# Performance work log

Measured on AMD Instinct MI355X. Metric: run time of the kernel, lower is better.

## Reference

```python
import jax, jax.numpy as jnp
import numpy as np

N_NODES = 50000
N_EDGES = 800000
IN_DIM = 128
HID_DIM = 256
N_CLASS = 40
PROP_STEP = 3
DROPOUT = 0.0  # eval-mode drop_node scale = (1 - DROPOUT)


def setup_inputs() -> dict:
    key = jax.random.key(0)
    k = jax.random.split(key, 6)
    features = jax.random.normal(k[0], (N_NODES, IN_DIM), dtype=jnp.float32)
    src = jax.random.randint(k[1], (N_EDGES,), 0, N_NODES)
    dst = jax.random.randint(k[2], (N_EDGES,), 0, N_NODES)
    W1 = jax.random.normal(k[3], (IN_DIM, HID_DIM), dtype=jnp.float32) / np.sqrt(IN_DIM)
    b1 = jnp.zeros((HID_DIM,), dtype=jnp.float32)
    W2 = jax.random.normal(k[4], (HID_DIM, N_CLASS), dtype=jnp.float32) / np.sqrt(HID_DIM)
    b2 = jnp.zeros((N_CLASS,), dtype=jnp.float32)
    return {"features": features, "src": src, "dst": dst,
            "W1": W1, "b1": b1, "W2": W2, "b2": b2}


def reference(features, src, dst, W1, b1, W2, b2):
    N = features.shape[0]
    # in-degree-based symmetric normalization: norm = deg^{-1/2}, deg clamped to >= 1
    degs = jax.ops.segment_sum(jnp.ones_like(dst, dtype=jnp.float32), dst,
                               num_segments=N)
    norm = jnp.clip(degs, 1.0, None) ** -0.5              # [N]
    w = norm[src] * norm[dst]                             # [E] edge weights (u_mul_v)

    # eval-mode drop_node: scale features by (1 - drop_rate)
    x = features * (1.0 - DROPOUT)
    y = x
    for _ in range(PROP_STEP):
        # u_mul_e: gather source features, scale by edge weight, scatter-sum to dst
        m = x[src] * w[:, None]                           # [E, F]
        x = jax.ops.segment_sum(m, dst, num_segments=N)   # [N, F]
        y = y + x
    feat = y / (PROP_STEP + 1)

    # MLP (use_bn=False, dropouts are 0 / eval): relu(linear) -> linear
    h = jax.nn.relu(feat @ W1 + b1)
    logits = h @ W2 + b2
    return jax.nn.log_softmax(logits, axis=-1)
```

## Files before the change

kernel.cpp:

```cpp
#include <hip/hip_runtime.h>

#define IN_DIM 128
#define HID    256
#define NCLS   40
#define BSHIFT 8
#define BSZ    256
#define MAXNB  256
#define CHUNK  4096
#define CAP    5120

static inline size_t align256(size_t x) { return (x + 255) & ~(size_t)255; }

typedef __attribute__((ext_vector_type(2))) float f32x2;

__device__ inline unsigned pack_bf16x2(float x, float y) {
    unsigned xb = __float_as_uint(x), yb = __float_as_uint(y);
    unsigned lo = (xb + 0x7fffu + ((xb >> 16) & 1u)) >> 16;
    unsigned hi = (yb + 0x7fffu + ((yb >> 16) & 1u)) >> 16;
    return lo | (hi << 16);
}
__device__ inline unsigned short f2bf(float x) {
    unsigned b = __float_as_uint(x);
    return (unsigned short)((b + 0x7fffu + ((b >> 16) & 1u)) >> 16);
}

__device__ inline unsigned pack_fp8x4(float a, float b, float c, float d) {
    int v = __builtin_amdgcn_cvt_pk_fp8_f32(a, b, 0, false);
    v = __builtin_amdgcn_cvt_pk_fp8_f32(c, d, v, true);
    return (unsigned)v;
}

__global__ __launch_bounds__(256) void init_kernel(
        int* __restrict__ cursor,
        const float* __restrict__ W1, const float* __restrict__ W2,
        unsigned short* __restrict__ W1T, unsigned short* __restrict__ W2T) {
    int i = blockIdx.x * 256 + threadIdx.x;
    if (i < MAXNB) cursor[i] = i * CAP;
    if (i < 256 * 128) {
        int n = i >> 7, k = i & 127;
        W1T[i] = f2bf(W1[k * 256 + n]);
    }
    if (i < 48 * 256) {
        int c = i >> 8, kk = i & 255;
        W2T[i] = (c < 40) ? f2bf(W2[kk * 40 + c]) : (unsigned short)0;
    }
}

__global__ __launch_bounds__(256) void bucket_scatter_kernel(
        const int* __restrict__ src, const int* __restrict__ dst,
        int* __restrict__ bucketCursor, unsigned* __restrict__ ebuf, int E) {
    __shared__ int hist[MAXNB], lofs[MAXNB], lcur[MAXNB], gbase[MAXNB];
    __shared__ unsigned bin[CHUNK];
    int t = threadIdx.x, lane = t & 63, wave = t >> 6;
    int start = blockIdx.x * CHUNK;
    int cnt = min(CHUNK, E - start);
    hist[t] = 0;
    __syncthreads();
    for (int i = t; i < cnt; i += 256) atomicAdd(&hist[dst[start + i] >> BSHIFT], 1);
    __syncthreads();
    int v = hist[t];
    int s = v;
    for (int off = 1; off < 64; off <<= 1) {
        int u = __shfl_up(s, off, 64);
        if (lane >= off) s += u;
    }
    __shared__ int wsum[4];
    if (lane == 63) wsum[wave] = s;
    __syncthreads();
    if (t == 0) {
        int c = 0;
        for (int i = 0; i < 4; ++i) { int x = wsum[i]; wsum[i] = c; c += x; }
    }
    __syncthreads();
    int excl = wsum[wave] + s - v;
    lofs[t] = excl; lcur[t] = excl;
    if (v) gbase[t] = atomicAdd(&bucketCursor[t], v);
    __syncthreads();
    for (int i = t; i < cnt; i += 256) {
        unsigned s0 = (unsigned)src[start + i], d0 = (unsigned)dst[start + i];
        int b = d0 >> BSHIFT;
        int r = atomicAdd(&lcur[b], 1);
        bin[r] = ((unsigned)b << 24) | ((d0 & (BSZ - 1)) << 16) | s0;
    }
    __syncthreads();
    for (int i = t; i < cnt; i += 256) {
        unsigned e = bin[i];
        int b = e >> 24;
        ebuf[gbase[b] + i - lofs[b]] = e;
    }
}

__global__ __launch_bounds__(256) void bucketize_kernel(
        const unsigned* __restrict__ ebuf, const int* __restrict__ bucketCursor,
        int* __restrict__ offs, int* __restrict__ degs,
        float* __restrict__ norm, float* __restrict__ sqn,
        unsigned short* __restrict__ csrS, int N) {
    __shared__ unsigned sedge[CAP];
    __shared__ unsigned short sout[CAP];
    __shared__ int hist[BSZ], lcur[BSZ];
    __shared__ int wsum[4];
    int b = blockIdx.x, t = threadIdx.x, lane = t & 63, wave = t >> 6;
    int base = b * CAP;
    int cnt = bucketCursor[b] - base;
    hist[t] = 0;
    __syncthreads();
    for (int i = t; i < cnt; i += 256) {
        unsigned e = ebuf[base + i];
        sedge[i] = e;
        atomicAdd(&hist[(e >> 16) & (BSZ - 1)], 1);
    }
    __syncthreads();
    int v = hist[t];
    int s = v;
    for (int off = 1; off < 64; off <<= 1) {
        int u = __shfl_up(s, off, 64);
        if (lane >= off) s += u;
    }
    if (lane == 63) wsum[wave] = s;
    __syncthreads();
    if (t == 0) {
        int c = 0;
        for (int i = 0; i < 4; ++i) { int x = wsum[i]; wsum[i] = c; c += x; }
    }
    __syncthreads();
    int excl = wsum[wave] + s - v;
    lcur[t] = excl;
    int node = b * BSZ + t;
    if (node < N) {
        offs[node] = base + excl;
        degs[node] = v;
        float dc = (float)(v > 0 ? v : 1);
        norm[node] = rsqrtf(dc);
        sqn[node] = sqrtf(dc);
    }
    __syncthreads();
    for (int i = t; i < cnt; i += 256) {
        unsigned e = sedge[i];
        int ld = (e >> 16) & (BSZ - 1);
        int p = atomicAdd(&lcur[ld], 1);
        sout[p] = (unsigned short)(e & 0xffffu);
    }
    __syncthreads();
    for (int i = t; i < cnt; i += 256) csrS[base + i] = sout[i];
}

__global__ __launch_bounds__(256) void prep_kernel(
        const float* __restrict__ feat, const float* __restrict__ norm,
        unsigned* __restrict__ x0, int nfeat_dw) {
    int i = blockIdx.x * 256 + threadIdx.x;
    if (i >= nfeat_dw) return;
    float s = norm[i >> 5];
    float4 f = *(const float4*)(feat + (size_t)i * 4);
    x0[i] = pack_fp8x4(f.x * s, f.y * s, f.z * s, f.w * s);
}

#define ACCP16(dd, ww)                                                        \
    {                                                                         \
        f32x2 wv2 = {(ww), (ww)};                                             \
        c0 += __builtin_amdgcn_cvt_pk_f32_fp8((int)(dd).x, false) * wv2;      \
        c1 += __builtin_amdgcn_cvt_pk_f32_fp8((int)(dd).x, true ) * wv2;      \
        c2 += __builtin_amdgcn_cvt_pk_f32_fp8((int)(dd).y, false) * wv2;      \
        c3 += __builtin_amdgcn_cvt_pk_f32_fp8((int)(dd).y, true ) * wv2;      \
        c4 += __builtin_amdgcn_cvt_pk_f32_fp8((int)(dd).z, false) * wv2;      \
        c5 += __builtin_amdgcn_cvt_pk_f32_fp8((int)(dd).z, true ) * wv2;      \
        c6 += __builtin_amdgcn_cvt_pk_f32_fp8((int)(dd).w, false) * wv2;      \
        c7 += __builtin_amdgcn_cvt_pk_f32_fp8((int)(dd).w, true ) * wv2;      \
    }

#define RED2(a) { a += __shfl_xor(a, 8, 64); a += __shfl_xor(a, 16, 64); }

__global__ __launch_bounds__(256) void prop_kernel(
        const unsigned* __restrict__ xin, unsigned* __restrict__ xout,
        const int* __restrict__ offs, const int* __restrict__ degs,
        const float* __restrict__ norm, const unsigned short* __restrict__ csrS, int N) {
    int t = threadIdx.x;
    int wv = t >> 6, lane = t & 63;
    int h = lane >> 5, hl = lane & 31;
    int g = hl >> 3, gl = hl & 7;
    int v = blockIdx.x * 8 + wv * 2 + h;
    if (v >= N) return;
    int start = offs[v], end = start + degs[v];
    f32x2 c0 = {0.f,0.f}, c1 = {0.f,0.f}, c2 = {0.f,0.f}, c3 = {0.f,0.f};
    f32x2 c4 = {0.f,0.f}, c5 = {0.f,0.f}, c6 = {0.f,0.f}, c7 = {0.f,0.f};
    for (int k = start; k < end; k += 16) {
        int cnt = min(16, end - k);
        if (cnt == 16) {
            uint4 d[4];
#pragma unroll
            for (int u = 0; u < 4; ++u) {
                int sx = (int)csrS[k + 4 * u + g];
                d[u] = *(const uint4*)(xin + (size_t)sx * 32 + gl * 4);
            }
#pragma unroll
            for (int u = 0; u < 4; ++u) ACCP16(d[u], 1.0f);
        } else if (cnt > 8) {
            uint4 d[4]; float w[4];
#pragma unroll
            for (int u = 0; u < 4; ++u) {
                int il = 4 * u + g;
                int sx = (int)csrS[k + min(il, cnt - 1)];
                w[u] = (il < cnt) ? 1.f : 0.f;
                d[u] = *(const uint4*)(xin + (size_t)sx * 32 + gl * 4);
            }
#pragma unroll
            for (int u = 0; u < 4; ++u) ACCP16(d[u], w[u]);
        } else {
            uint4 d[2]; float w[2];
#pragma unroll
            for (int u = 0; u < 2; ++u) {
                int il = 4 * u + g;
                int sx = (int)csrS[k + min(il, cnt - 1)];
                w[u] = (il < cnt) ? 1.f : 0.f;
                d[u] = *(const uint4*)(xin + (size_t)sx * 32 + gl * 4);
            }
#pragma unroll
            for (int u = 0; u < 2; ++u) ACCP16(d[u], w[u]);
        }
    }
    float a0 = c0.x, a1 = c0.y, a2 = c1.x, a3 = c1.y;
    float a4 = c2.x, a5 = c2.y, a6 = c3.x, a7 = c3.y;
    float a8 = c4.x, a9 = c4.y, a10 = c5.x, a11 = c5.y;
    float a12 = c6.x, a13 = c6.y, a14 = c7.x, a15 = c7.y;
    RED2(a0); RED2(a1); RED2(a2); RED2(a3); RED2(a4); RED2(a5); RED2(a6); RED2(a7);
    RED2(a8); RED2(a9); RED2(a10); RED2(a11); RED2(a12); RED2(a13); RED2(a14); RED2(a15);
    if (g == 0) {
        float nv = norm[v];
        float s2 = nv * nv;
        uint4 o;
        o.x = pack_fp8x4(a0 * s2, a1 * s2, a2 * s2, a3 * s2);
        o.y = pack_fp8x4(a4 * s2, a5 * s2, a6 * s2, a7 * s2);
        o.z = pack_fp8x4(a8 * s2, a9 * s2, a10 * s2, a11 * s2);
        o.w = pack_fp8x4(a12 * s2, a13 * s2, a14 * s2, a15 * s2);
        *(uint4*)(xout + (size_t)v * 32 + gl * 4) = o;
    }
}

typedef __attribute__((ext_vector_type(8))) short bf16x8;
typedef __attribute__((ext_vector_type(4))) float f32x4;

#define SA_STRIDE 136
#define SH_STRIDE 264

__device__ inline void unpack8(uint2 u, float* q) {
    f32x2 p;
    p = __builtin_amdgcn_cvt_pk_f32_fp8((int)u.x, false); q[0] = p.x; q[1] = p.y;
    p = __builtin_amdgcn_cvt_pk_f32_fp8((int)u.x, true ); q[2] = p.x; q[3] = p.y;
    p = __builtin_amdgcn_cvt_pk_f32_fp8((int)u.y, false); q[4] = p.x; q[5] = p.y;
    p = __builtin_amdgcn_cvt_pk_f32_fp8((int)u.y, true ); q[6] = p.x; q[7] = p.y;
}

__global__ __launch_bounds__(256) void mlp16_kernel(
        const unsigned* __restrict__ x0, const unsigned* __restrict__ x1,
        const unsigned* __restrict__ x2, const unsigned* __restrict__ x3,
        const float* __restrict__ sqn,
        const unsigned short* __restrict__ W1T, const float* __restrict__ b1,
        const unsigned short* __restrict__ W2T, const float* __restrict__ b2,
        float* __restrict__ out, int N) {
    __shared__ unsigned short sA[16 * SA_STRIDE];
    __shared__ unsigned short sH[16 * SH_STRIDE];
    __shared__ float sLog[16][49];
    int t = threadIdx.x, wv = t >> 6, lane = t & 63;
    int l15 = lane & 15, lq = lane >> 4;
    int base = blockIdx.x * 16;

    {
        int n = t >> 4, sg = t & 15;
        int gv = base + n;
        uint4 o = make_uint4(0u, 0u, 0u, 0u);
        if (gv < N) {
            size_t xo = (size_t)gv * 32 + sg * 2;
            uint2 u0 = *(const uint2*)(x0 + xo);
            uint2 u1 = *(const uint2*)(x1 + xo);
            uint2 u2 = *(const uint2*)(x2 + xo);
            uint2 u3 = *(const uint2*)(x3 + xo);
            float q0[8], q1[8], q2[8], q3[8];
            unpack8(u0, q0); unpack8(u1, q1); unpack8(u2, q2); unpack8(u3, q3);
            float fac = 0.25f * sqn[gv];
            float s[8];
#pragma unroll
            for (int i = 0; i < 8; ++i) s[i] = (q0[i] + q1[i] + q2[i] + q3[i]) * fac;
            o.x = pack_bf16x2(s[0], s[1]); o.y = pack_bf16x2(s[2], s[3]);
            o.z = pack_bf16x2(s[4], s[5]); o.w = pack_bf16x2(s[6], s[7]);
        }
        *(uint4*)&sA[n * SA_STRIDE + sg * 8] = o;
    }
    __syncthreads();

    f32x4 acc[4];
#pragma unroll
    for (int ht = 0; ht < 4; ++ht) acc[ht] = (f32x4){0.f, 0.f, 0.f, 0.f};
#pragma unroll
    for (int s = 0; s < 4; ++s) {
        bf16x8 afr = *(const bf16x8*)&sA[l15 * SA_STRIDE + s * 32 + lq * 8];
#pragma unroll
        for (int ht = 0; ht < 4; ++ht) {
            bf16x8 bfr = *(const bf16x8*)(W1T + ((wv * 64 + ht * 16 + l15) * 128 + s * 32 + lq * 8));
            acc[ht] = __builtin_amdgcn_mfma_f32_16x16x32_bf16(afr, bfr, acc[ht], 0, 0, 0);
        }
    }
#pragma unroll
    for (int ht = 0; ht < 4; ++ht) {
        int hid = wv * 64 + ht * 16 + l15;
        float bb = b1[hid];
#pragma unroll
        for (int r = 0; r < 4; ++r) {
            int node = lq * 4 + r;
            sH[node * SH_STRIDE + hid] = f2bf(fmaxf(acc[ht][r] + bb, 0.f));
        }
    }
    __syncthreads();

    if (wv < 3) {
        int ct = wv;
        f32x4 acc2 = (f32x4){0.f, 0.f, 0.f, 0.f};
#pragma unroll
        for (int s = 0; s < 8; ++s) {
            bf16x8 afr = *(const bf16x8*)&sH[l15 * SH_STRIDE + s * 32 + lq * 8];
            bf16x8 bfr = *(const bf16x8*)(W2T + ((ct * 16 + l15) * 256 + s * 32 + lq * 8));
            acc2 = __builtin_amdgcn_mfma_f32_16x16x32_bf16(afr, bfr, acc2, 0, 0, 0);
        }
        int c = ct * 16 + l15;
        float bb = (c < NCLS) ? b2[c] : 0.f;
#pragma unroll
        for (int r = 0; r < 4; ++r) sLog[lq * 4 + r][c] = acc2[r] + bb;
    }
    __syncthreads();
    if (wv != 0) return;

    float lg[3][4];
#pragma unroll
    for (int ct = 0; ct < 3; ++ct)
#pragma unroll
        for (int r = 0; r < 4; ++r) lg[ct][r] = sLog[lq * 4 + r][ct * 16 + l15];
#pragma unroll
    for (int r = 0; r < 4; ++r) {
        float m = fmaxf(lg[0][r], lg[1][r]);
        if (l15 < 8) m = fmaxf(m, lg[2][r]);
        for (int off = 1; off < 16; off <<= 1) m = fmaxf(m, __shfl_xor(m, off, 64));
        float ssum = __expf(lg[0][r] - m) + __expf(lg[1][r] - m) +
                     ((l15 < 8) ? __expf(lg[2][r] - m) : 0.f);
        for (int off = 1; off < 16; off <<= 1) ssum += __shfl_xor(ssum, off, 64);
        float ls = m + __logf(ssum);
        int node = base + lq * 4 + r;
        if (node < N) {
#pragma unroll
            for (int ct = 0; ct < 3; ++ct) {
                int c = ct * 16 + l15;
                if (c < NCLS) out[(size_t)node * NCLS + c] = lg[ct][r] - ls;
            }
        }
    }
}

extern "C" void kernel_launch(void* const* d_in, const int* in_sizes, int n_in,
                              void* d_out, int out_size, void* d_ws, size_t ws_size,
                              hipStream_t stream) {
    const float* feat = (const float*)d_in[0];
    const int*   src  = (const int*)d_in[1];
    const int*   dst  = (const int*)d_in[2];
    const float* W1   = (const float*)d_in[3];
    const float* b1   = (const float*)d_in[4];
    const float* W2   = (const float*)d_in[5];
    const float* b2   = (const float*)d_in[6];
    float* out = (float*)d_out;

    int N = in_sizes[0] / IN_DIM;
    int E = in_sizes[1];
    int NB = (N + BSZ - 1) / BSZ;

    char* ws = (char*)d_ws;
    size_t off = 0;
    float* norm   = (float*)(ws + off); off += align256((size_t)N * 4);
    float* sqn    = (float*)(ws + off); off += align256((size_t)N * 4);
    int*   offs   = (int*)(ws + off);   off += align256((size_t)N * 4);
    int*   degs   = (int*)(ws + off);   off += align256((size_t)N * 4);
    int*   bCur   = (int*)(ws + off);   off += align256((size_t)MAXNB * 4);
    unsigned* ebuf = (unsigned*)(ws + off); off += align256((size_t)MAXNB * CAP * 4);
    unsigned short* csrS = (unsigned short*)(ws + off); off += align256((size_t)MAXNB * CAP * 2);
    unsigned* x0  = (unsigned*)(ws + off); off += align256((size_t)N * 32 * 4);
    unsigned* x1  = (unsigned*)(ws + off); off += align256((size_t)N * 32 * 4);
    unsigned* x2  = (unsigned*)(ws + off); off += align256((size_t)N * 32 * 4);
    unsigned* x3  = (unsigned*)(ws + off); off += align256((size_t)N * 32 * 4);
    unsigned short* W1T = (unsigned short*)(ws + off); off += align256((size_t)256 * 128 * 2);
    unsigned short* W2T = (unsigned short*)(ws + off); off += align256((size_t)48 * 256 * 2);
    (void)ws_size;

    init_kernel<<<128, 256, 0, stream>>>(bCur, W1, W2, W1T, W2T);

    int echunks = (E + CHUNK - 1) / CHUNK;
    bucket_scatter_kernel<<<echunks, 256, 0, stream>>>(src, dst, bCur, ebuf, E);
    bucketize_kernel<<<NB, 256, 0, stream>>>(ebuf, bCur, offs, degs, norm, sqn, csrS, N);

    prep_kernel<<<(N * 32 + 255) / 256, 256, 0, stream>>>(feat, norm, x0, N * 32);

    int pb = (N + 7) / 8;
    prop_kernel<<<pb, 256, 0, stream>>>(x0, x1, offs, degs, norm, csrS, N);
    prop_kernel<<<pb, 256, 0, stream>>>(x1, x2, offs, degs, norm, csrS, N);
    prop_kernel<<<pb, 256, 0, stream>>>(x2, x3, offs, degs, norm, csrS, N);

    mlp16_kernel<<<(N + 15) / 16, 256, 0, stream>>>(x0, x1, x2, x3, sqn,
                                                    W1T, b1, W2T, b2, out, N);
}
```

Measured before the change: 221.7 us.

## Fuse three propagation steps into a persistent kernel with grid barriers

Replaces the three separate prop_kernel launches with one persistent kernel of 1024 blocks that loops over node groups and uses an atomic-counter grid barrier between steps. It also folds the feature prep (norm scaling and fp8 packing) into the tail of the bucketize kernel. The aim is to remove launch overhead and inter-kernel gaps. In exchange, a spin-wait barrier is added that relies on all 1024 blocks being co-resident, which is a deadlock risk if occupancy is lower. The persistent grid-stride loop may also balance work less well than the full launch did.

```diff
diff --git a/kernel.cpp b/kernel.cpp
--- a/kernel.cpp
+++ b/kernel.cpp
@@ -8,10 +8,13 @@
 #define MAXNB  256
 #define CHUNK  4096
 #define CAP    5120
+#define P3GRID 1024
 
 static inline size_t align256(size_t x) { return (x + 255) & ~(size_t)255; }
 
 typedef __attribute__((ext_vector_type(2))) float f32x2;
+typedef __attribute__((ext_vector_type(8))) short bf16x8;
+typedef __attribute__((ext_vector_type(4))) float f32x4;
 
 __device__ inline unsigned pack_bf16x2(float x, float y) {
     unsigned xb = __float_as_uint(x), yb = __float_as_uint(y);
@@ -31,11 +34,12 @@
 }
 
 __global__ __launch_bounds__(256) void init_kernel(
-        int* __restrict__ cursor,
+        int* __restrict__ cursor, int* __restrict__ bar,
         const float* __restrict__ W1, const float* __restrict__ W2,
         unsigned short* __restrict__ W1T, unsigned short* __restrict__ W2T) {
     int i = blockIdx.x * 256 + threadIdx.x;
     if (i < MAXNB) cursor[i] = i * CAP;
+    if (i < 4) bar[i] = 0;
     if (i < 256 * 128) {
         int n = i >> 7, k = i & 127;
         W1T[i] = f2bf(W1[k * 256 + n]);
@@ -94,10 +98,12 @@
         const unsigned* __restrict__ ebuf, const int* __restrict__ bucketCursor,
         int* __restrict__ offs, int* __restrict__ degs,
         float* __restrict__ norm, float* __restrict__ sqn,
-        unsigned short* __restrict__ csrS, int N) {
+        unsigned short* __restrict__ csrS,
+        const float* __restrict__ feat, unsigned* __restrict__ x0, int N) {
     __shared__ unsigned sedge[CAP];
     __shared__ unsigned short sout[CAP];
     __shared__ int hist[BSZ], lcur[BSZ];
+    __shared__ float snorm[BSZ];
     __shared__ int wsum[4];
     int b = blockIdx.x, t = threadIdx.x, lane = t & 63, wave = t >> 6;
     int base = b * CAP;
@@ -126,13 +132,16 @@
     int excl = wsum[wave] + s - v;
     lcur[t] = excl;
     int node = b * BSZ + t;
+    float nv = 0.f;
     if (node < N) {
         offs[node] = base + excl;
         degs[node] = v;
         float dc = (float)(v > 0 ? v : 1);
-        norm[node] = rsqrtf(dc);
+        nv = rsqrtf(dc);
+        norm[node] = nv;
         sqn[node] = sqrtf(dc);
     }
+    snorm[t] = nv;
     __syncthreads();
     for (int i = t; i < cnt; i += 256) {
         unsigned e = sedge[i];
@@ -142,16 +151,18 @@
     }
     __syncthreads();
     for (int i = t; i < cnt; i += 256) csrS[base + i] = sout[i];
-}
-
-__global__ __launch_bounds__(256) void prep_kernel(
-        const float* __restrict__ feat, const float* __restrict__ norm,
-        unsigned* __restrict__ x0, int nfeat_dw) {
-    int i = blockIdx.x * 256 + threadIdx.x;
-    if (i >= nfeat_dw) return;
-    float s = norm[i >> 5];
-    float4 f = *(const float4*)(feat + (size_t)i * 4);
-    x0[i] = pack_fp8x4(f.x * s, f.y * s, f.z * s, f.w * s);
+
+    int nbase = b * BSZ;
+    int nvalid = min(BSZ, N - nbase);
+    if (nvalid <= 0) return;
+    int total = nvalid * 32;
+    const float4* f4 = (const float4*)(feat + (size_t)nbase * IN_DIM);
+    unsigned* xo = x0 + (size_t)nbase * 32;
+    for (int i = t; i < total; i += 256) {
+        float sc = snorm[i >> 5];
+        float4 f = f4[i];
+        xo[i] = pack_fp8x4(f.x * sc, f.y * sc, f.z * sc, f.w * sc);
+    }
 }
 
 #define ACCP16(dd, ww)                                                        \
@@ -169,74 +180,102 @@
 
 #define RED2(a) { a += __shfl_xor(a, 8, 64); a += __shfl_xor(a, 16, 64); }
 
-__global__ __launch_bounds__(256) void prop_kernel(
-        const unsigned* __restrict__ xin, unsigned* __restrict__ xout,
+__device__ inline void grid_barrier(int* bar, int slot, int nblk) {
+    __syncthreads();
+    if (threadIdx.x == 0) {
+        __threadfence();
+        atomicAdd(&bar[slot], 1);
+        while (__hip_atomic_load(&bar[slot], __ATOMIC_ACQUIRE,
+                                 __HIP_MEMORY_SCOPE_AGENT) < nblk) {
+            __builtin_amdgcn_s_sleep(1);
+        }
+        __threadfence();
+    }
+    __syncthreads();
+}
+
+__global__ __launch_bounds__(256, 4) void prop3_kernel(
+        const unsigned* __restrict__ x0, unsigned* __restrict__ x1,
+        unsigned* __restrict__ x2, unsigned* __restrict__ x3,
         const int* __restrict__ offs, const int* __restrict__ degs,
-        const float* __restrict__ norm, const unsigned short* __restrict__ csrS, int N) {
+        const float* __restrict__ norm, const unsigned short* __restrict__ csrS,
+        int* __restrict__ bar, int N) {
     int t = threadIdx.x;
     int wv = t >> 6, lane = t & 63;
     int h = lane >> 5, hl = lane & 31;
     int g = hl >> 3, gl = hl & 7;
-    int v = blockIdx.x * 8 + wv * 2 + h;
-    if (v >= N) return;
-    int start = offs[v], end = start + degs[v];
-    f32x2 c0 = {0.f,0.f}, c1 = {0.f,0.f}, c2 = {0.f,0.f}, c3 = {0.f,0.f};
-    f32x2 c4 = {0.f,0.f}, c5 = {0.f,0.f}, c6 = {0.f,0.f}, c7 = {0.f,0.f};
-    for (int k = start; k < end; k += 16) {
-        int cnt = min(16, end - k);
-        if (cnt == 16) {
-            uint4 d[4];
-#pragma unroll
-            for (int u = 0; u < 4; ++u) {
-                int sx = (int)csrS[k + 4 * u + g];
-                d[u] = *(const uint4*)(xin + (size_t)sx * 32 + gl * 4);
+    (void)hl;
+    int ngrp = (N + 7) >> 3;
+
+    const unsigned* xin = x0;
+    unsigned* xout = x1;
+    for (int step = 0; step < 3; ++step) {
+        for (int grp = blockIdx.x; grp < ngrp; grp += gridDim.x) {
+            int v = grp * 8 + wv * 2 + h;
+            if (v < N) {
+                float nv = norm[v];
+                int start = offs[v], end = start + degs[v];
+                f32x2 c0 = {0.f,0.f}, c1 = {0.f,0.f}, c2 = {0.f,0.f}, c3 = {0.f,0.f};
+                f32x2 c4 = {0.f,0.f}, c5 = {0.f,0.f}, c6 = {0.f,0.f}, c7 = {0.f,0.f};
+                for (int k = start; k < end; k += 16) {
+                    int cnt = min(16, end - k);
+                    if (cnt == 16) {
+                        uint4 d[4];
+#pragma unroll
+                        for (int u = 0; u < 4; ++u) {
+                            int sx = (int)csrS[k + 4 * u + g];
+                            d[u] = *(const uint4*)(xin + (size_t)sx * 32 + gl * 4);
+                        }
+#pragma unroll
+                        for (int u = 0; u < 4; ++u) ACCP16(d[u], 1.0f);
+                    } else if (cnt > 8) {
+                        uint4 d[4]; float w[4];
+#pragma unroll
+                        for (int u = 0; u < 4; ++u) {
+                            int il = 4 * u + g;
+                            int sx = (int)csrS[k + min(il, cnt - 1)];
+                            w[u] = (il < cnt) ? 1.f : 0.f;
+                            d[u] = *(const uint4*)(xin + (size_t)sx * 32 + gl * 4);
+                        }
+#pragma unroll
+                        for (int u = 0; u < 4; ++u) ACCP16(d[u], w[u]);
+                    } else {
+                        uint4 d[2]; float w[2];
+#pragma unroll
+                        for (int u = 0; u < 2; ++u) {
+                            int il = 4 * u + g;
+                            int sx = (int)csrS[k + min(il, cnt - 1)];
+                            w[u] = (il < cnt) ? 1.f : 0.f;
+                            d[u] = *(const uint4*)(xin + (size_t)sx * 32 + gl * 4);
+                        }
+#pragma unroll
+                        for (int u = 0; u < 2; ++u) ACCP16(d[u], w[u]);
+                    }
+                }
+                float a0 = c0.x, a1 = c0.y, a2 = c1.x, a3 = c1.y;
+                float a4 = c2.x, a5 = c2.y, a6 = c3.x, a7 = c3.y;
+                float a8 = c4.x, a9 = c4.y, a10 = c5.x, a11 = c5.y;
+                float a12 = c6.x, a13 = c6.y, a14 = c7.x, a15 = c7.y;
+                RED2(a0); RED2(a1); RED2(a2); RED2(a3);
+                RED2(a4); RED2(a5); RED2(a6); RED2(a7);
+                RED2(a8); RED2(a9); RED2(a10); RED2(a11);
+                RED2(a12); RED2(a13); RED2(a14); RED2(a15);
+                if (g == 0) {
+                    float s2 = nv * nv;
+                    uint4 o;
+                    o.x = pack_fp8x4(a0 * s2, a1 * s2, a2 * s2, a3 * s2);
+                    o.y = pack_fp8x4(a4 * s2, a5 * s2, a6 * s2, a7 * s2);
+                    o.z = pack_fp8x4(a8 * s2, a9 * s2, a10 * s2, a11 * s2);
+                    o.w = pack_fp8x4(a12 * s2, a13 * s2, a14 * s2, a15 * s2);
+                    *(uint4*)(xout + (size_t)v * 32 + gl * 4) = o;
+                }
             }
-#pragma unroll
-            for (int u = 0; u < 4; ++u) ACCP16(d[u], 1.0f);
-        } else if (cnt > 8) {
-            uint4 d[4]; float w[4];
-#pragma unroll
-            for (int u = 0; u < 4; ++u) {
-                int il = 4 * u + g;
-                int sx = (int)csrS[k + min(il, cnt - 1)];
-                w[u] = (il < cnt) ? 1.f : 0.f;
-                d[u] = *(const uint4*)(xin + (size_t)sx * 32 + gl * 4);
-            }
-#pragma unroll
-            for (int u = 0; u < 4; ++u) ACCP16(d[u], w[u]);
-        } else {
-            uint4 d[2]; float w[2];
-#pragma unroll
-            for (int u = 0; u < 2; ++u) {
-                int il = 4 * u + g;
-                int sx = (int)csrS[k + min(il, cnt - 1)];
-                w[u] = (il < cnt) ? 1.f : 0.f;
-                d[u] = *(const uint4*)(xin + (size_t)sx * 32 + gl * 4);
-            }
-#pragma unroll
-            for (int u = 0; u < 2; ++u) ACCP16(d[u], w[u]);
-        }
-    }
-    float a0 = c0.x, a1 = c0.y, a2 = c1.x, a3 = c1.y;
-    float a4 = c2.x, a5 = c2.y, a6 = c3.x, a7 = c3.y;
-    float a8 = c4.x, a9 = c4.y, a10 = c5.x, a11 = c5.y;
-    float a12 = c6.x, a13 = c6.y, a14 = c7.x, a15 = c7.y;
-    RED2(a0); RED2(a1); RED2(a2); RED2(a3); RED2(a4); RED2(a5); RED2(a6); RED2(a7);
-    RED2(a8); RED2(a9); RED2(a10); RED2(a11); RED2(a12); RED2(a13); RED2(a14); RED2(a15);
-    if (g == 0) {
-        float nv = norm[v];
-        float s2 = nv * nv;
-        uint4 o;
-        o.x = pack_fp8x4(a0 * s2, a1 * s2, a2 * s2, a3 * s2);
-        o.y = pack_fp8x4(a4 * s2, a5 * s2, a6 * s2, a7 * s2);
-        o.z = pack_fp8x4(a8 * s2, a9 * s2, a10 * s2, a11 * s2);
-        o.w = pack_fp8x4(a12 * s2, a13 * s2, a14 * s2, a15 * s2);
-        *(uint4*)(xout + (size_t)v * 32 + gl * 4) = o;
-    }
-}
-
-typedef __attribute__((ext_vector_type(8))) short bf16x8;
-typedef __attribute__((ext_vector_type(4))) float f32x4;
+        }
+        if (step < 2) grid_barrier(bar, step, (int)gridDim.x);
+        xin  = (step == 0) ? (const unsigned*)x1 : (const unsigned*)x2;
+        xout = (step == 0) ? x2 : x3;
+    }
+}
 
 #define SA_STRIDE 136
 #define SH_STRIDE 264
@@ -375,6 +414,7 @@
     int*   offs   = (int*)(ws + off);   off += align256((size_t)N * 4);
     int*   degs   = (int*)(ws + off);   off += align256((size_t)N * 4);
     int*   bCur   = (int*)(ws + off);   off += align256((size_t)MAXNB * 4);
+    int*   bar    = (int*)(ws + off);   off += align256((size_t)4 * 4);
     unsigned* ebuf = (unsigned*)(ws + off); off += align256((size_t)MAXNB * CAP * 4);
     unsigned short* csrS = (unsigned short*)(ws + off); off += align256((size_t)MAXNB * CAP * 2);
     unsigned* x0  = (unsigned*)(ws + off); off += align256((size_t)N * 32 * 4);
@@ -385,18 +425,15 @@
     unsigned short* W2T = (unsigned short*)(ws + off); off += align256((size_t)48 * 256 * 2);
     (void)ws_size;
 
-    init_kernel<<<128, 256, 0, stream>>>(bCur, W1, W2, W1T, W2T);
+    init_kernel<<<128, 256, 0, stream>>>(bCur, bar, W1, W2, W1T, W2T);
 
     int echunks = (E + CHUNK - 1) / CHUNK;
     bucket_scatter_kernel<<<echunks, 256, 0, stream>>>(src, dst, bCur, ebuf, E);
-    bucketize_kernel<<<NB, 256, 0, stream>>>(ebuf, bCur, offs, degs, norm, sqn, csrS, N);
-
-    prep_kernel<<<(N * 32 + 255) / 256, 256, 0, stream>>>(feat, norm, x0, N * 32);
-
-    int pb = (N + 7) / 8;
-    prop_kernel<<<pb, 256, 0, stream>>>(x0, x1, offs, degs, norm, csrS, N);
-    prop_kernel<<<pb, 256, 0, stream>>>(x1, x2, offs, degs, norm, csrS, N);
-    prop_kernel<<<pb, 256, 0, stream>>>(x2, x3, offs, degs, norm, csrS, N);
+    bucketize_kernel<<<NB, 256, 0, stream>>>(ebuf, bCur, offs, degs, norm, sqn, csrS,
+                                             feat, x0, N);
+
+    prop3_kernel<<<P3GRID, 256, 0, stream>>>(x0, x1, x2, x3, offs, degs, norm,
+                                             csrS, bar, N);
 
     mlp16_kernel<<<(N + 15) / 16, 256, 0, stream>>>(x0, x1, x2, x3, sqn,
                                                     W1T, b1, W2T, b2, out, N);
```

Result: slower. 616.8 us (+178.3%).

## Split fp8 feature rows into two half-planes and fold prep into bucketize

Applied to the files above, without the earlier changes.

Feature buffers now use two planes of 64 fp8 values per node instead of one 128-byte row. Each propagation wave makes two passes over a node's neighbours, one per plane, with 8 edges gathered in parallel by 4-lane groups. The goal is to shrink the working set per pass so it stays in cache, and to widen edge-level parallelism. The separate prep kernel is folded into bucketize to save a launch and a norm read, and output stores become nontemporal. The cost is reading the CSR indices twice and a three-step shuffle reduction instead of two.

```diff
diff --git a/kernel.cpp b/kernel.cpp
--- a/kernel.cpp
+++ b/kernel.cpp
@@ -12,6 +12,9 @@
 static inline size_t align256(size_t x) { return (x + 255) & ~(size_t)255; }
 
 typedef __attribute__((ext_vector_type(2))) float f32x2;
+typedef __attribute__((ext_vector_type(8))) short bf16x8;
+typedef __attribute__((ext_vector_type(4))) float f32x4;
+typedef __attribute__((ext_vector_type(4))) unsigned u32x4;
 
 __device__ inline unsigned pack_bf16x2(float x, float y) {
     unsigned xb = __float_as_uint(x), yb = __float_as_uint(y);
@@ -94,10 +97,12 @@
         const unsigned* __restrict__ ebuf, const int* __restrict__ bucketCursor,
         int* __restrict__ offs, int* __restrict__ degs,
         float* __restrict__ norm, float* __restrict__ sqn,
-        unsigned short* __restrict__ csrS, int N) {
+        unsigned short* __restrict__ csrS,
+        const float* __restrict__ feat, unsigned* __restrict__ x0, int N) {
     __shared__ unsigned sedge[CAP];
     __shared__ unsigned short sout[CAP];
     __shared__ int hist[BSZ], lcur[BSZ];
+    __shared__ float snorm[BSZ];
     __shared__ int wsum[4];
     int b = blockIdx.x, t = threadIdx.x, lane = t & 63, wave = t >> 6;
     int base = b * CAP;
@@ -126,13 +131,16 @@
     int excl = wsum[wave] + s - v;
     lcur[t] = excl;
     int node = b * BSZ + t;
+    float nv = 0.f;
     if (node < N) {
         offs[node] = base + excl;
         degs[node] = v;
         float dc = (float)(v > 0 ? v : 1);
-        norm[node] = rsqrtf(dc);
+        nv = rsqrtf(dc);
+        norm[node] = nv;
         sqn[node] = sqrtf(dc);
     }
+    snorm[t] = nv;
     __syncthreads();
     for (int i = t; i < cnt; i += 256) {
         unsigned e = sedge[i];
@@ -142,16 +150,20 @@
     }
     __syncthreads();
     for (int i = t; i < cnt; i += 256) csrS[base + i] = sout[i];
-}
-
-__global__ __launch_bounds__(256) void prep_kernel(
-        const float* __restrict__ feat, const float* __restrict__ norm,
-        unsigned* __restrict__ x0, int nfeat_dw) {
-    int i = blockIdx.x * 256 + threadIdx.x;
-    if (i >= nfeat_dw) return;
-    float s = norm[i >> 5];
-    float4 f = *(const float4*)(feat + (size_t)i * 4);
-    x0[i] = pack_fp8x4(f.x * s, f.y * s, f.z * s, f.w * s);
+
+    int nbase = b * BSZ;
+    int nvalid = min(BSZ, N - nbase);
+    if (nvalid <= 0) return;
+    int total = nvalid * 32;
+    size_t plane = (size_t)N * 16;
+    const float4* f4 = (const float4*)(feat + (size_t)nbase * IN_DIM);
+    for (int i = t; i < total; i += 256) {
+        float sc = snorm[i >> 5];
+        float4 f = f4[i];
+        unsigned pk = pack_fp8x4(f.x * sc, f.y * sc, f.z * sc, f.w * sc);
+        int n = i >> 5, j = i & 31;
+        x0[(size_t)(j >> 4) * plane + (size_t)(nbase + n) * 16 + (j & 15)] = pk;
+    }
 }
 
 #define ACCP16(dd, ww)                                                        \
@@ -167,7 +179,7 @@
         c7 += __builtin_amdgcn_cvt_pk_f32_fp8((int)(dd).w, true ) * wv2;      \
     }
 
-#define RED2(a) { a += __shfl_xor(a, 8, 64); a += __shfl_xor(a, 16, 64); }
+#define RED3(a) { a += __shfl_xor(a, 4, 64); a += __shfl_xor(a, 8, 64); a += __shfl_xor(a, 16, 64); }
 
 __global__ __launch_bounds__(256) void prop_kernel(
         const unsigned* __restrict__ xin, unsigned* __restrict__ xout,
@@ -176,67 +188,64 @@
     int t = threadIdx.x;
     int wv = t >> 6, lane = t & 63;
     int h = lane >> 5, hl = lane & 31;
-    int g = hl >> 3, gl = hl & 7;
+    int g = hl >> 2, gl = hl & 3;
     int v = blockIdx.x * 8 + wv * 2 + h;
     if (v >= N) return;
     int start = offs[v], end = start + degs[v];
-    f32x2 c0 = {0.f,0.f}, c1 = {0.f,0.f}, c2 = {0.f,0.f}, c3 = {0.f,0.f};
-    f32x2 c4 = {0.f,0.f}, c5 = {0.f,0.f}, c6 = {0.f,0.f}, c7 = {0.f,0.f};
-    for (int k = start; k < end; k += 16) {
-        int cnt = min(16, end - k);
-        if (cnt == 16) {
-            uint4 d[4];
-#pragma unroll
-            for (int u = 0; u < 4; ++u) {
-                int sx = (int)csrS[k + 4 * u + g];
-                d[u] = *(const uint4*)(xin + (size_t)sx * 32 + gl * 4);
+    float nv = norm[v];
+    float s2 = nv * nv;
+    size_t plane = (size_t)N * 16;
+#pragma unroll
+    for (int p = 0; p < 2; ++p) {
+        const unsigned* xp = xin + (size_t)p * plane;
+        f32x2 c0 = {0.f,0.f}, c1 = {0.f,0.f}, c2 = {0.f,0.f}, c3 = {0.f,0.f};
+        f32x2 c4 = {0.f,0.f}, c5 = {0.f,0.f}, c6 = {0.f,0.f}, c7 = {0.f,0.f};
+        for (int k = start; k < end; k += 32) {
+            int cnt = min(32, end - k);
+            if (cnt == 32) {
+                uint4 d[4];
+#pragma unroll
+                for (int u = 0; u < 4; ++u) {
+                    int sx = (int)csrS[k + u * 8 + g];
+                    d[u] = *(const uint4*)(xp + (size_t)sx * 16 + gl * 4);
+                }
+#pragma unroll
+                for (int u = 0; u < 4; ++u) ACCP16(d[u], 1.0f);
+            } else {
+                int nb = (cnt + 7) >> 3;
+                uint4 d[4]; float w[4];
+#pragma unroll
+                for (int u = 0; u < 4; ++u) {
+                    if (u < nb) {
+                        int il = u * 8 + g;
+                        int sx = (int)csrS[k + min(il, cnt - 1)];
+                        w[u] = (il < cnt) ? 1.f : 0.f;
+                        d[u] = *(const uint4*)(xp + (size_t)sx * 16 + gl * 4);
+                    }
+                }
+#pragma unroll
+                for (int u = 0; u < 4; ++u) if (u < nb) ACCP16(d[u], w[u]);
             }
-#pragma unroll
-            for (int u = 0; u < 4; ++u) ACCP16(d[u], 1.0f);
-        } else if (cnt > 8) {
-            uint4 d[4]; float w[4];
-#pragma unroll
-            for (int u = 0; u < 4; ++u) {
-                int il = 4 * u + g;
-                int sx = (int)csrS[k + min(il, cnt - 1)];
-                w[u] = (il < cnt) ? 1.f : 0.f;
-                d[u] = *(const uint4*)(xin + (size_t)sx * 32 + gl * 4);
-            }
-#pragma unroll
-            for (int u = 0; u < 4; ++u) ACCP16(d[u], w[u]);
-        } else {
-            uint4 d[2]; float w[2];
-#pragma unroll
-            for (int u = 0; u < 2; ++u) {
-                int il = 4 * u + g;
-                int sx = (int)csrS[k + min(il, cnt - 1)];
-                w[u] = (il < cnt) ? 1.f : 0.f;
-                d[u] = *(const uint4*)(xin + (size_t)sx * 32 + gl * 4);
-            }
-#pragma unroll
-            for (int u = 0; u < 2; ++u) ACCP16(d[u], w[u]);
-        }
-    }
-    float a0 = c0.x, a1 = c0.y, a2 = c1.x, a3 = c1.y;
-    float a4 = c2.x, a5 = c2.y, a6 = c3.x, a7 = c3.y;
-    float a8 = c4.x, a9 = c4.y, a10 = c5.x, a11 = c5.y;
-    float a12 = c6.x, a13 = c6.y, a14 = c7.x, a15 = c7.y;
-    RED2(a0); RED2(a1); RED2(a2); RED2(a3); RED2(a4); RED2(a5); RED2(a6); RED2(a7);
-    RED2(a8); RED2(a9); RED2(a10); RED2(a11); RED2(a12); RED2(a13); RED2(a14); RED2(a15);
-    if (g == 0) {
-        float nv = norm[v];
-        float s2 = nv * nv;
-        uint4 o;
-        o.x = pack_fp8x4(a0 * s2, a1 * s2, a2 * s2, a3 * s2);
-        o.y = pack_fp8x4(a4 * s2, a5 * s2, a6 * s2, a7 * s2);
-        o.z = pack_fp8x4(a8 * s2, a9 * s2, a10 * s2, a11 * s2);
-        o.w = pack_fp8x4(a12 * s2, a13 * s2, a14 * s2, a15 * s2);
-        *(uint4*)(xout + (size_t)v * 32 + gl * 4) = o;
-    }
-}
-
-typedef __attribute__((ext_vector_type(8))) short bf16x8;
-typedef __attribute__((ext_vector_type(4))) float f32x4;
+        }
+        float a0 = c0.x, a1 = c0.y, a2 = c1.x, a3 = c1.y;
+        float a4 = c2.x, a5 = c2.y, a6 = c3.x, a7 = c3.y;
+        float a8 = c4.x, a9 = c4.y, a10 = c5.x, a11 = c5.y;
+        float a12 = c6.x, a13 = c6.y, a14 = c7.x, a15 = c7.y;
+        RED3(a0); RED3(a1); RED3(a2); RED3(a3);
+        RED3(a4); RED3(a5); RED3(a6); RED3(a7);
+        RED3(a8); RED3(a9); RED3(a10); RED3(a11);
+        RED3(a12); RED3(a13); RED3(a14); RED3(a15);
+        if (g == 0) {
+            u32x4 o;
+            o.x = pack_fp8x4(a0 * s2, a1 * s2, a2 * s2, a3 * s2);
+            o.y = pack_fp8x4(a4 * s2, a5 * s2, a6 * s2, a7 * s2);
+            o.z = pack_fp8x4(a8 * s2, a9 * s2, a10 * s2, a11 * s2);
+            o.w = pack_fp8x4(a12 * s2, a13 * s2, a14 * s2, a15 * s2);
+            __builtin_nontemporal_store(
+                o, (u32x4*)(xout + (size_t)p * plane + (size_t)v * 16 + gl * 4));
+        }
+    }
+}
 
 #define SA_STRIDE 136
 #define SH_STRIDE 264
@@ -268,7 +277,7 @@
         int gv = base + n;
         uint4 o = make_uint4(0u, 0u, 0u, 0u);
         if (gv < N) {
-            size_t xo = (size_t)gv * 32 + sg * 2;
+            size_t xo = (size_t)(sg >> 3) * (size_t)N * 16 + (size_t)gv * 16 + (sg & 7) * 2;
             uint2 u0 = *(const uint2*)(x0 + xo);
             uint2 u1 = *(const uint2*)(x1 + xo);
             uint2 u2 = *(const uint2*)(x2 + xo);
@@ -282,7 +291,7 @@
             o.x = pack_bf16x2(s[0], s[1]); o.y = pack_bf16x2(s[2], s[3]);
             o.z = pack_bf16x2(s[4], s[5]); o.w = pack_bf16x2(s[6], s[7]);
         }
-        *(uint4*)&sA[n * SA_STRIDE + sg * 8] = o;
+        *(uint4*)&sA[(t >> 4) * SA_STRIDE + (t & 15) * 8] = o;
     }
     __syncthreads();
 
@@ -389,9 +398,8 @@
 
     int echunks = (E + CHUNK - 1) / CHUNK;
     bucket_scatter_kernel<<<echunks, 256, 0, stream>>>(src, dst, bCur, ebuf, E);
-    bucketize_kernel<<<NB, 256, 0, stream>>>(ebuf, bCur, offs, degs, norm, sqn, csrS, N);
-
-    prep_kernel<<<(N * 32 + 255) / 256, 256, 0, stream>>>(feat, norm, x0, N * 32);
+    bucketize_kernel<<<NB, 256, 0, stream>>>(ebuf, bCur, offs, degs, norm, sqn, csrS,
+                                             feat, x0, N);
 
     int pb = (N + 7) / 8;
     prop_kernel<<<pb, 256, 0, stream>>>(x0, x1, offs, degs, norm, csrS, N);
```

Result: slower. 285.4 us (+28.8%).

## Fuse feature prep into bucketize and process four nodes per half-wave in prop

Applied to the files above, without the earlier changes.

The fp8 pre-scaling of input features now happens at the end of bucketize_kernel, using norms held in shared memory, so the separate prep kernel launch and its global norm reads are gone. prop_kernel now has each half-wave handle four consecutive destination nodes in a loop, cutting the grid size by four. This trims launch count and per-block overhead. The cost is less parallelism in prop and a longer tail in bucketize, which now uses only about 196 blocks to stream the feature matrix.

```diff
diff --git a/kernel.cpp b/kernel.cpp
--- a/kernel.cpp
+++ b/kernel.cpp
@@ -12,6 +12,8 @@
 static inline size_t align256(size_t x) { return (x + 255) & ~(size_t)255; }
 
 typedef __attribute__((ext_vector_type(2))) float f32x2;
+typedef __attribute__((ext_vector_type(8))) short bf16x8;
+typedef __attribute__((ext_vector_type(4))) float f32x4;
 
 __device__ inline unsigned pack_bf16x2(float x, float y) {
     unsigned xb = __float_as_uint(x), yb = __float_as_uint(y);
@@ -94,10 +96,12 @@
         const unsigned* __restrict__ ebuf, const int* __restrict__ bucketCursor,
         int* __restrict__ offs, int* __restrict__ degs,
         float* __restrict__ norm, float* __restrict__ sqn,
-        unsigned short* __restrict__ csrS, int N) {
+        unsigned short* __restrict__ csrS,
+        const float* __restrict__ feat, unsigned* __restrict__ x0, int N) {
     __shared__ unsigned sedge[CAP];
     __shared__ unsigned short sout[CAP];
     __shared__ int hist[BSZ], lcur[BSZ];
+    __shared__ float snorm[BSZ];
     __shared__ int wsum[4];
     int b = blockIdx.x, t = threadIdx.x, lane = t & 63, wave = t >> 6;
     int base = b * CAP;
@@ -126,13 +130,16 @@
     int excl = wsum[wave] + s - v;
     lcur[t] = excl;
     int node = b * BSZ + t;
+    float nv = 0.f;
     if (node < N) {
         offs[node] = base + excl;
         degs[node] = v;
         float dc = (float)(v > 0 ? v : 1);
-        norm[node] = rsqrtf(dc);
+        nv = rsqrtf(dc);
+        norm[node] = nv;
         sqn[node] = sqrtf(dc);
     }
+    snorm[t] = nv;
     __syncthreads();
     for (int i = t; i < cnt; i += 256) {
         unsigned e = sedge[i];
@@ -142,16 +149,18 @@
     }
     __syncthreads();
     for (int i = t; i < cnt; i += 256) csrS[base + i] = sout[i];
-}
-
-__global__ __launch_bounds__(256) void prep_kernel(
-        const float* __restrict__ feat, const float* __restrict__ norm,
-        unsigned* __restrict__ x0, int nfeat_dw) {
-    int i = blockIdx.x * 256 + threadIdx.x;
-    if (i >= nfeat_dw) return;
-    float s = norm[i >> 5];
-    float4 f = *(const float4*)(feat + (size_t)i * 4);
-    x0[i] = pack_fp8x4(f.x * s, f.y * s, f.z * s, f.w * s);
+
+    int nbase = b * BSZ;
+    int nvalid = min(BSZ, N - nbase);
+    if (nvalid <= 0) return;
+    int total = nvalid * 32;
+    const float4* f4 = (const float4*)(feat + (size_t)nbase * IN_DIM);
+    unsigned* xo = x0 + (size_t)nbase * 32;
+    for (int i = t; i < total; i += 256) {
+        float sc = snorm[i >> 5];
+        float4 f = f4[i];
+        xo[i] = pack_fp8x4(f.x * sc, f.y * sc, f.z * sc, f.w * sc);
+    }
 }
 
 #define ACCP16(dd, ww)                                                        \
@@ -177,66 +186,68 @@
     int wv = t >> 6, lane = t & 63;
     int h = lane >> 5, hl = lane & 31;
     int g = hl >> 3, gl = hl & 7;
-    int v = blockIdx.x * 8 + wv * 2 + h;
-    if (v >= N) return;
-    int start = offs[v], end = start + degs[v];
-    f32x2 c0 = {0.f,0.f}, c1 = {0.f,0.f}, c2 = {0.f,0.f}, c3 = {0.f,0.f};
-    f32x2 c4 = {0.f,0.f}, c5 = {0.f,0.f}, c6 = {0.f,0.f}, c7 = {0.f,0.f};
-    for (int k = start; k < end; k += 16) {
-        int cnt = min(16, end - k);
-        if (cnt == 16) {
-            uint4 d[4];
-#pragma unroll
-            for (int u = 0; u < 4; ++u) {
-                int sx = (int)csrS[k + 4 * u + g];
-                d[u] = *(const uint4*)(xin + (size_t)sx * 32 + gl * 4);
+    int v0 = blockIdx.x * 32 + (wv * 2 + h) * 4;
+    for (int vi = 0; vi < 4; ++vi) {
+        int v = v0 + vi;
+        if (v >= N) break;
+        int start = offs[v], end = start + degs[v];
+        f32x2 c0 = {0.f,0.f}, c1 = {0.f,0.f}, c2 = {0.f,0.f}, c3 = {0.f,0.f};
+        f32x2 c4 = {0.f,0.f}, c5 = {0.f,0.f}, c6 = {0.f,0.f}, c7 = {0.f,0.f};
+        for (int k = start; k < end; k += 16) {
+            int cnt = min(16, end - k);
+            if (cnt == 16) {
+                uint4 d[4];
+#pragma unroll
+                for (int u = 0; u < 4; ++u) {
+                    int sx = (int)csrS[k + 4 * u + g];
+                    d[u] = *(const uint4*)(xin + (size_t)sx * 32 + gl * 4);
+                }
+#pragma unroll
+                for (int u = 0; u < 4; ++u) ACCP16(d[u], 1.0f);
+            } else if (cnt > 8) {
+                uint4 d[4]; float w[4];
+#pragma unroll
+                for (int u = 0; u < 4; ++u) {
+                    int il = 4 * u + g;
+                    int sx = (int)csrS[k + min(il, cnt - 1)];
+                    w[u] = (il < cnt) ? 1.f : 0.f;
+                    d[u] = *(const uint4*)(xin + (size_t)sx * 32 + gl * 4);
+                }
+#pragma unroll
+                for (int u = 0; u < 4; ++u) ACCP16(d[u], w[u]);
+            } else {
+                uint4 d[2]; float w[2];
+#pragma unroll
+                for (int u = 0; u < 2; ++u) {
+                    int il = 4 * u + g;
+                    int sx = (int)csrS[k + min(il, cnt - 1)];
+                    w[u] = (il < cnt) ? 1.f : 0.f;
+                    d[u] = *(const uint4*)(xin + (size_t)sx * 32 + gl * 4);
+                }
+#pragma unroll
+                for (int u = 0; u < 2; ++u) ACCP16(d[u], w[u]);
             }
-#pragma unroll
-            for (int u = 0; u < 4; ++u) ACCP16(d[u], 1.0f);
-        } else if (cnt > 8) {
-            uint4 d[4]; float w[4];
-#pragma unroll
-            for (int u = 0; u < 4; ++u) {
-                int il = 4 * u + g;
-                int sx = (int)csrS[k + min(il, cnt - 1)];
-                w[u] = (il < cnt) ? 1.f : 0.f;
-                d[u] = *(const uint4*)(xin + (size_t)sx * 32 + gl * 4);
-            }
-#pragma unroll
-            for (int u = 0; u < 4; ++u) ACCP16(d[u], w[u]);
-        } else {
-            uint4 d[2]; float w[2];
-#pragma unroll
-            for (int u = 0; u < 2; ++u) {
-                int il = 4 * u + g;
-                int sx = (int)csrS[k + min(il, cnt - 1)];
-                w[u] = (il < cnt) ? 1.f : 0.f;
-                d[u] = *(const uint4*)(xin + (size_t)sx * 32 + gl * 4);
-            }
-#pragma unroll
-            for (int u = 0; u < 2; ++u) ACCP16(d[u], w[u]);
-        }
-    }
-    float a0 = c0.x, a1 = c0.y, a2 = c1.x, a3 = c1.y;
-    float a4 = c2.x, a5 = c2.y, a6 = c3.x, a7 = c3.y;
-    float a8 = c4.x, a9 = c4.y, a10 = c5.x, a11 = c5.y;
-    float a12 = c6.x, a13 = c6.y, a14 = c7.x, a15 = c7.y;
-    RED2(a0); RED2(a1); RED2(a2); RED2(a3); RED2(a4); RED2(a5); RED2(a6); RED2(a7);
-    RED2(a8); RED2(a9); RED2(a10); RED2(a11); RED2(a12); RED2(a13); RED2(a14); RED2(a15);
-    if (g == 0) {
-        float nv = norm[v];
-        float s2 = nv * nv;
-        uint4 o;
-        o.x = pack_fp8x4(a0 * s2, a1 * s2, a2 * s2, a3 * s2);
-        o.y = pack_fp8x4(a4 * s2, a5 * s2, a6 * s2, a7 * s2);
-        o.z = pack_fp8x4(a8 * s2, a9 * s2, a10 * s2, a11 * s2);
-        o.w = pack_fp8x4(a12 * s2, a13 * s2, a14 * s2, a15 * s2);
-        *(uint4*)(xout + (size_t)v * 32 + gl * 4) = o;
-    }
-}
-
-typedef __attribute__((ext_vector_type(8))) short bf16x8;
-typedef __attribute__((ext_vector_type(4))) float f32x4;
+        }
+        float a0 = c0.x, a1 = c0.y, a2 = c1.x, a3 = c1.y;
+        float a4 = c2.x, a5 = c2.y, a6 = c3.x, a7 = c3.y;
+        float a8 = c4.x, a9 = c4.y, a10 = c5.x, a11 = c5.y;
+        float a12 = c6.x, a13 = c6.y, a14 = c7.x, a15 = c7.y;
+        RED2(a0); RED2(a1); RED2(a2); RED2(a3);
+        RED2(a4); RED2(a5); RED2(a6); RED2(a7);
+        RED2(a8); RED2(a9); RED2(a10); RED2(a11);
+        RED2(a12); RED2(a13); RED2(a14); RED2(a15);
+        if (g == 0) {
+            float nv = norm[v];
+            float s2 = nv * nv;
+            uint4 o;
+            o.x = pack_fp8x4(a0 * s2, a1 * s2, a2 * s2, a3 * s2);
+            o.y = pack_fp8x4(a4 * s2, a5 * s2, a6 * s2, a7 * s2);
+            o.z = pack_fp8x4(a8 * s2, a9 * s2, a10 * s2, a11 * s2);
+            o.w = pack_fp8x4(a12 * s2, a13 * s2, a14 * s2, a15 * s2);
+            *(uint4*)(xout + (size_t)v * 32 + gl * 4) = o;
+        }
+    }
+}
 
 #define SA_STRIDE 136
 #define SH_STRIDE 264
@@ -389,11 +400,10 @@
 
     int echunks = (E + CHUNK - 1) / CHUNK;
     bucket_scatter_kernel<<<echunks, 256, 0, stream>>>(src, dst, bCur, ebuf, E);
-    bucketize_kernel<<<NB, 256, 0, stream>>>(ebuf, bCur, offs, degs, norm, sqn, csrS, N);
-
-    prep_kernel<<<(N * 32 + 255) / 256, 256, 0, stream>>>(feat, norm, x0, N * 32);
-
-    int pb = (N + 7) / 8;
+    bucketize_kernel<<<NB, 256, 0, stream>>>(ebuf, bCur, offs, degs, norm, sqn, csrS,
+                                             feat, x0, N);
+
+    int pb = (N + 31) / 32;
     prop_kernel<<<pb, 256, 0, stream>>>(x0, x1, offs, degs, norm, csrS, N);
     prop_kernel<<<pb, 256, 0, stream>>>(x1, x2, offs, degs, norm, csrS, N);
     prop_kernel<<<pb, 256, 0, stream>>>(x2, x3, offs, degs, norm, csrS, N);
```

New measurement: 255.8 us. 15.4% more time.
